# Performance work log

Hardware: AMD Instinct MI355X
Metric: run time of the kernel (lower is better)

Reference implementation:

```python
import jax, jax.numpy as jnp
import numpy as np

N, E, FIN, H, G, L = 100000, 300000, 128, 256, 4000, 5
BN_EPS = 1e-5

def setup_inputs() -> dict:
    key = jax.random.key(0)
    ks = jax.random.split(key, 24)
    s = 0.05
    inp = {
        "x": jax.random.normal(ks[0], (N, FIN), dtype=jnp.float32),
        "edge_index": jax.random.randint(ks[1], (2, E), 0, N, dtype=jnp.int64),
        "batch": jnp.sort(jax.random.randint(ks[2], (N,), 0, G, dtype=jnp.int64)),
        # input projection
        "in_W": jax.random.normal(ks[3], (FIN, H), dtype=jnp.float32) * s,
        "in_b": jnp.zeros((H,), dtype=jnp.float32),
        # stacked per-layer GIN MLP params (Linear-BN-ReLU-Linear-BN-ReLU)
        "conv_W1": jax.random.normal(ks[4], (L, H, H), dtype=jnp.float32) * s,
        "conv_b1": jnp.zeros((L, H), dtype=jnp.float32),
        "conv_g1": jnp.ones((L, H), dtype=jnp.float32),
        "conv_be1": jnp.zeros((L, H), dtype=jnp.float32),
        "conv_W2": jax.random.normal(ks[5], (L, H, H), dtype=jnp.float32) * s,
        "conv_b2": jnp.zeros((L, H), dtype=jnp.float32),
        "conv_g2": jnp.ones((L, H), dtype=jnp.float32),
        "conv_be2": jnp.zeros((L, H), dtype=jnp.float32),
        "eps": jnp.zeros((L,), dtype=jnp.float32),
        # head MLP
        "head_W1": jax.random.normal(ks[6], (H, H // 2), dtype=jnp.float32) * s,
        "head_b1": jnp.zeros((H // 2,), dtype=jnp.float32),
        "head_W2": jax.random.normal(ks[7], (H // 2, 1), dtype=jnp.float32) * s,
        "head_b2": jnp.zeros((1,), dtype=jnp.float32),
    }
    return inp

def _bn(h, g, b):
    # BatchNorm1d over node dim (training-mode batch stats)
    m = jnp.mean(h, axis=0)
    v = jnp.var(h, axis=0)
    return g * (h - m) * jax.lax.rsqrt(v + BN_EPS) + b

def reference(x, edge_index, batch, in_W, in_b, conv_W1, conv_b1, conv_g1,
              conv_be1, conv_W2, conv_b2, conv_g2, conv_be2, eps,
              head_W1, head_b1, head_W2, head_b2):
    src, dst = edge_index[0], edge_index[1]
    h = jax.nn.relu(x @ in_W + in_b)  # [N,H]
    for l in range(L):
        agg = jax.ops.segment_sum(h[src], dst, num_segments=N)  # scatter-add
        z = (1.0 + eps[l]) * h + agg
        z = jax.nn.relu(_bn(z @ conv_W1[l] + conv_b1[l], conv_g1[l], conv_be1[l]))
        h = jax.nn.relu(_bn(z @ conv_W2[l] + conv_b2[l], conv_g2[l], conv_be2[l]))
        # dropout is identity in eval/reference
    # global mean pool by graph id
    sums = jax.ops.segment_sum(h, batch, num_segments=G)  # [G,H]
    cnt = jax.ops.segment_sum(jnp.ones((N,), h.dtype), batch, num_segments=G)
    pooled = sums / jnp.maximum(cnt, 1.0)[:, None]
    hid = jax.nn.relu(pooled @ head_W1 + head_b1)
    return hid @ head_W2 + head_b2  # [G,1]
```

## Files before the change

kernel.cpp:

```cpp
#include <hip/hip_runtime.h>
#include <hip/hip_bf16.h>
#include <stdint.h>
#include <stddef.h>

#define NN 100000
#define NE 300000
#define FINDIM 128
#define HD 256
#define NG 4000
#define NLAYER 5
#define MPAD 100096
#define NT (MPAD/32)
#define MG 384

typedef __attribute__((ext_vector_type(8))) short bf8;
typedef __attribute__((ext_vector_type(4))) float f4;

#define FENCE() __asm__ volatile("" ::: "memory")
#define WAITVM0() __asm__ volatile("s_waitcnt vmcnt(0)" ::: "memory")
#define WAITVM4() __asm__ volatile("s_waitcnt vmcnt(4)" ::: "memory")
#define WAITVM6() __asm__ volatile("s_waitcnt vmcnt(6)" ::: "memory")
#define WAITLGKM() __asm__ volatile("s_waitcnt lgkmcnt(0)" ::: "memory")
#define BARRIER() do { FENCE(); __builtin_amdgcn_s_barrier(); FENCE(); } while(0)

__device__ __forceinline__ unsigned short f2bf(float f){
  union { float f; unsigned u; } uf; uf.f = f;
  unsigned r = uf.u + 0x7fffu + ((uf.u >> 16) & 1u);
  return (unsigned short)(r >> 16);
}
__device__ __forceinline__ float bf2f(unsigned short h){
  union { unsigned u; float f; } uf; uf.u = ((unsigned)h) << 16; return uf.f;
}

__device__ __forceinline__ void gload16(const void* g, void* l){
  __builtin_amdgcn_global_load_lds((const __attribute__((address_space(1))) void*)g,
                                   (__attribute__((address_space(3))) void*)l, 16, 0, 0);
}

__global__ void k_zero(int* __restrict__ p, int n){
  int i = blockIdx.x*256 + threadIdx.x;
  if(i < n) p[i] = 0;
}

__global__ void k_count(const int* __restrict__ ei, int* __restrict__ counts){
  int e = blockIdx.x*256 + threadIdx.x;
  if(e < NE) atomicAdd(&counts[ei[NE + e]], 1);
}

__global__ void k_scan_partial(const int* __restrict__ counts, int* __restrict__ partials){
  __shared__ int sw[4];
  int b = blockIdx.x, t = threadIdx.x;
  int base = b*1024 + t*4;
  int s = 0;
  #pragma unroll
  for(int j=0;j<4;j++){ int i = base+j; if(i < NN) s += counts[i]; }
  #pragma unroll
  for(int d=1; d<64; d<<=1) s += __shfl_xor(s, d, 64);
  if((t & 63) == 0) sw[t>>6] = s;
  __syncthreads();
  if(t == 0) partials[b] = sw[0]+sw[1]+sw[2]+sw[3];
}

__global__ void k_scan_tot(int* __restrict__ partials, int* __restrict__ offsets, int nb){
  __shared__ int sm[128];
  int t = threadIdx.x;
  int v = (t < nb) ? partials[t] : 0;
  sm[t] = v; __syncthreads();
  for(int d=1; d<128; d<<=1){
    int x = 0;
    if(t >= d) x = sm[t-d];
    __syncthreads();
    sm[t] += x;
    __syncthreads();
  }
  if(t < nb) partials[t] = sm[t] - v;
  if(t == 127) offsets[NN] = sm[127];
}

__global__ void k_scan_final(const int* __restrict__ counts, const int* __restrict__ partials,
                             int* __restrict__ offsets, int* __restrict__ cursor){
  __shared__ int wsum[4];
  int b = blockIdx.x, t = threadIdx.x;
  int base = b*1024 + t*4;
  int c[4]; int ts = 0;
  #pragma unroll
  for(int j=0;j<4;j++){ int i = base+j; c[j] = (i < NN) ? counts[i] : 0; ts += c[j]; }
  int lane = t & 63;
  int inc = ts;
  #pragma unroll
  for(int d=1; d<64; d<<=1){ int x = __shfl_up(inc, d, 64); if(lane >= d) inc += x; }
  if(lane == 63) wsum[t>>6] = inc;
  __syncthreads();
  int woff = 0;
  for(int w2=0; w2<(t>>6); w2++) woff += wsum[w2];
  int excl = partials[b] + woff + inc - ts;
  #pragma unroll
  for(int j=0;j<4;j++){
    int i = base+j;
    if(i < NN){ offsets[i] = excl; cursor[i] = excl; excl += c[j]; }
  }
}

__global__ void k_fill(const int* __restrict__ ei, int* __restrict__ cursor, int* __restrict__ eidx){
  int e = blockIdx.x*256 + threadIdx.x;
  if(e < NE){
    int d = ei[NE + e];
    int pos = atomicAdd(&cursor[d], 1);
    eidx[pos] = ei[e];
  }
}

__global__ void k_wt(const float* __restrict__ src, unsigned short* __restrict__ dst, int K, int Ncols){
  int l = blockIdx.y;
  size_t base = (size_t)l * K * Ncols;
  int i = blockIdx.x*256 + threadIdx.x;
  if(i < K*Ncols){
    int k = i / Ncols, n = i % Ncols;
    dst[base + (size_t)n*K + k] = f2bf(src[base + i]);
  }
}

template<int TRANS, bool RELUOUT, bool STATS>
__global__ __launch_bounds__(256, 3) void k_gemmb(
    const unsigned short* __restrict__ A, const unsigned short* __restrict__ Bt,
    const float* __restrict__ bias, const float* __restrict__ preS,
    const float* __restrict__ preT, unsigned short* __restrict__ C,
    float* __restrict__ stats)
{
  __shared__ __align__(16) unsigned short As[2][8192];
  __shared__ __align__(16) unsigned short Cs[4][1152];
  __shared__ __align__(16) float SP[512];
  const int t = threadIdx.x;
  const int lane = t & 63, w = t >> 6;
  const int q = lane >> 4, ln = lane & 15;
  const int nh = blockIdx.x & 1;
  const int mg = blockIdx.x >> 1;
  const int nbase = nh*128 + w*32;

  if(TRANS){ SP[t] = preS[t]; SP[256 + t] = preT[t]; WAITLGKM(); }

  bf8 bb[2][8];
  #pragma unroll
  for(int nf=0; nf<2; nf++)
    #pragma unroll
    for(int s=0; s<8; s++)
      bb[nf][s] = *(const bf8*)(Bt + (size_t)(nbase + nf*16 + ln)*HD + s*32 + q*8);

  float bv[2];
  #pragma unroll
  for(int nf=0; nf<2; nf++) bv[nf] = bias[nbase + nf*16 + ln];

  auto issueA = [&](int mt, int b){
    const int m0 = mt*32;
    #pragma unroll
    for(int j=0; j<4; j++){
      int slot = j*256 + t;
      int row = slot >> 5, p = slot & 31;
      int c = p ^ (row & 7);
      gload16(A + (size_t)(m0 + row)*HD + c*8, &As[b][(j*256 + w*64)*8]);
    }
  };

  float sacc[2] = {0.f, 0.f}, ssacc[2] = {0.f, 0.f};

  issueA(mg, 0);
  issueA(mg + MG, 1);

  int tc = 0;
  for(int mt = mg; mt < NT; mt += MG, tc++){
    const bool last = (mt + MG >= NT);
    if(last)           WAITVM0();
    else if(tc == 0)   WAITVM4();
    else               WAITVM6();
    BARRIER();

    unsigned short* Ab = &As[tc&1][0];
    const int m0 = mt*32;
    const bool padt = (m0 >= NN);

    if(TRANS){
      #pragma unroll
      for(int j=0; j<4; j++){
        int slot = j*256 + t;
        if(padt){
          *(uint4*)&Ab[slot*8] = (uint4){0u,0u,0u,0u};
        } else {
          int row = slot >> 5, p = slot & 31;
          int c = p ^ (row & 7);
          uint4 u = *(const uint4*)&Ab[slot*8];
          f4 s0 = *(const f4*)&SP[c*8];
          f4 s1 = *(const f4*)&SP[c*8 + 4];
          f4 t0 = *(const f4*)&SP[256 + c*8];
          f4 t1 = *(const f4*)&SP[256 + c*8 + 4];
          float scv[8] = {s0.x,s0.y,s0.z,s0.w,s1.x,s1.y,s1.z,s1.w};
          float shv[8] = {t0.x,t0.y,t0.z,t0.w,t1.x,t1.y,t1.z,t1.w};
          unsigned short* us = (unsigned short*)&u;
          #pragma unroll
          for(int e=0; e<8; e++){
            float v = bf2f(us[e]);
            v = fmaxf(fmaf(scv[e], v, shv[e]), 0.f);
            us[e] = f2bf(v);
          }
          *(uint4*)&Ab[slot*8] = u;
        }
      }
      WAITLGKM();
      BARRIER();
    }

    f4 acc[2][2];
    #pragma unroll
    for(int i=0;i<2;i++)
      #pragma unroll
      for(int j=0;j<2;j++) acc[i][j] = (f4){0.f,0.f,0.f,0.f};

    #pragma unroll
    for(int s=0; s<8; s++){
      bf8 af[2];
      #pragma unroll
      for(int mi=0; mi<2; mi++){
        int row = mi*16 + ln;
        int p = (s*4 + q) ^ (row & 7);
        af[mi] = *(const bf8*)&Ab[row*256 + p*8];
      }
      #pragma unroll
      for(int mi=0; mi<2; mi++)
        #pragma unroll
        for(int nf=0; nf<2; nf++)
          acc[mi][nf] = __builtin_amdgcn_mfma_f32_16x16x32_bf16(af[mi], bb[nf][s], acc[mi][nf], 0, 0, 0);
    }

    if(STATS){
      #pragma unroll
      for(int nf=0; nf<2; nf++)
        #pragma unroll
        for(int mi=0; mi<2; mi++)
          #pragma unroll
          for(int r=0; r<4; r++){
            float v = acc[mi][nf][r];
            sacc[nf] += v; ssacc[nf] = fmaf(v, v, ssacc[nf]);
          }
    }

    unsigned short* wsc = &Cs[w][0];
    #pragma unroll
    for(int mi=0; mi<2; mi++)
      #pragma unroll
      for(int nf=0; nf<2; nf++)
        #pragma unroll
        for(int r=0; r<4; r++){
          float v = acc[mi][nf][r] + bv[nf];
          if(RELUOUT) v = fmaxf(v, 0.f);
          if(padt) v = 0.f;
          wsc[(mi*16 + q*4 + r)*36 + nf*16 + ln] = f2bf(v);
        }
    {
      int r2 = lane >> 1, ch = lane & 1;
      size_t cb = (size_t)(m0 + r2)*HD + nh*128 + w*32;
      uint4 u0 = *(const uint4*)&wsc[r2*36 + ch*8];
      uint4 u1 = *(const uint4*)&wsc[r2*36 + (ch+2)*8];
      *(uint4*)&C[cb + ch*8]     = u0;
      *(uint4*)&C[cb + (ch+2)*8] = u1;
    }

    WAITLGKM();
    BARRIER();
    if(mt + 2*MG < NT) issueA(mt + 2*MG, tc&1);
  }

  if(STATS){
    #pragma unroll
    for(int nf=0; nf<2; nf++){
      float s = sacc[nf], ss = ssacc[nf];
      s  += __shfl_xor(s, 16, 64);  s  += __shfl_xor(s, 32, 64);
      ss += __shfl_xor(ss, 16, 64); ss += __shfl_xor(ss, 32, 64);
      if(q == 0){
        int gn = nbase + nf*16 + ln;
        atomicAdd(&stats[gn], s);
        atomicAdd(&stats[HD + gn], ss);
      }
    }
  }
}

__global__ __launch_bounds__(256, 3) void k_gemmb_in(
    const float* __restrict__ A, const unsigned short* __restrict__ Bt,
    const float* __restrict__ bias, unsigned short* __restrict__ C)
{
  __shared__ __align__(16) unsigned short As[4096];
  __shared__ __align__(16) unsigned short Cs[4][1152];
  const int t = threadIdx.x;
  const int lane = t & 63, w = t >> 6;
  const int q = lane >> 4, ln = lane & 15;
  const int nh = blockIdx.x & 1;
  const int mg = blockIdx.x >> 1;
  const int nbase = nh*128 + w*32;

  bf8 bb[2][4];
  #pragma unroll
  for(int nf=0; nf<2; nf++)
    #pragma unroll
    for(int s=0; s<4; s++)
      bb[nf][s] = *(const bf8*)(Bt + (size_t)(nbase + nf*16 + ln)*FINDIM + s*32 + q*8);

  float bv[2];
  #pragma unroll
  for(int nf=0; nf<2; nf++) bv[nf] = bias[nbase + nf*16 + ln];

  for(int mt = mg; mt < NT; mt += MG){
    const int m0 = mt*32;
    const bool padt = (m0 >= NN);
    __syncthreads();
    #pragma unroll
    for(int j=0; j<2; j++){
      int slot = j*256 + t;
      int row = slot >> 4, p = slot & 15;
      int c = p ^ (row & 7);
      int gm = m0 + row;
      f4 v0 = (f4){0.f,0.f,0.f,0.f}, v1 = (f4){0.f,0.f,0.f,0.f};
      if(gm < NN){
        v0 = *(const f4*)&A[(size_t)gm*FINDIM + c*8];
        v1 = *(const f4*)&A[(size_t)gm*FINDIM + c*8 + 4];
      }
      ushort4 a0, a1;
      a0.x = f2bf(v0.x); a0.y = f2bf(v0.y); a0.z = f2bf(v0.z); a0.w = f2bf(v0.w);
      a1.x = f2bf(v1.x); a1.y = f2bf(v1.y); a1.z = f2bf(v1.z); a1.w = f2bf(v1.w);
      *(ushort4*)&As[row*128 + p*8]     = a0;
      *(ushort4*)&As[row*128 + p*8 + 4] = a1;
    }
    __syncthreads();

    f4 acc[2][2];
    #pragma unroll
    for(int i=0;i<2;i++)
      #pragma unroll
      for(int j=0;j<2;j++) acc[i][j] = (f4){0.f,0.f,0.f,0.f};

    #pragma unroll
    for(int s=0; s<4; s++){
      bf8 af[2];
      #pragma unroll
      for(int mi=0; mi<2; mi++){
        int row = mi*16 + ln;
        int p = (s*4 + q) ^ (row & 7);
        af[mi] = *(const bf8*)&As[row*128 + p*8];
      }
      #pragma unroll
      for(int mi=0; mi<2; mi++)
        #pragma unroll
        for(int nf=0; nf<2; nf++)
          acc[mi][nf] = __builtin_amdgcn_mfma_f32_16x16x32_bf16(af[mi], bb[nf][s], acc[mi][nf], 0, 0, 0);
    }

    unsigned short* wsc = &Cs[w][0];
    #pragma unroll
    for(int mi=0; mi<2; mi++)
      #pragma unroll
      for(int nf=0; nf<2; nf++)
        #pragma unroll
        for(int r=0; r<4; r++){
          float v = fmaxf(acc[mi][nf][r] + bv[nf], 0.f);
          if(padt) v = 0.f;
          wsc[(mi*16 + q*4 + r)*36 + nf*16 + ln] = f2bf(v);
        }
    int r2 = lane >> 1, ch = lane & 1;
    size_t cb = (size_t)(m0 + r2)*HD + nh*128 + w*32;
    uint4 u0 = *(const uint4*)&wsc[r2*36 + ch*8];
    uint4 u1 = *(const uint4*)&wsc[r2*36 + (ch+2)*8];
    *(uint4*)&C[cb + ch*8]     = u0;
    *(uint4*)&C[cb + (ch+2)*8] = u1;
  }
}

__global__ void k_bnfin(const float* __restrict__ cs, const float* __restrict__ bias,
                        const float* __restrict__ g, const float* __restrict__ be,
                        float* __restrict__ sc, float* __restrict__ sh){
  int c = threadIdx.x;
  float m0 = cs[c] * (1.0f/NN);
  float mean = m0 + bias[c];
  float var  = cs[HD + c] * (1.0f/NN) - m0*m0;
  float s = g[c] * rsqrtf(var + 1e-5f);
  sc[c] = s;
  sh[c] = be[c] - mean*s;
}

__device__ __forceinline__ f4 act4(ushort4 uv, f4 s4, f4 t4, int ident){
  f4 u;
  u.x = bf2f(uv.x); u.y = bf2f(uv.y); u.z = bf2f(uv.z); u.w = bf2f(uv.w);
  if(!ident){
    u.x = fmaxf(fmaf(s4.x, u.x, t4.x), 0.f);
    u.y = fmaxf(fmaf(s4.y, u.y, t4.y), 0.f);
    u.z = fmaxf(fmaf(s4.z, u.z, t4.z), 0.f);
    u.w = fmaxf(fmaf(s4.w, u.w, t4.w), 0.f);
  }
  return u;
}

__global__ __launch_bounds__(256) void k_agg(const unsigned short* __restrict__ src,
    unsigned short* __restrict__ dst,
    const int* __restrict__ offs, const int* __restrict__ eidx,
    const float* __restrict__ eps, int l,
    const float* __restrict__ sc, const float* __restrict__ sh, int ident)
{
  int wv = threadIdx.x >> 6;
  int n = blockIdx.x*4 + wv;
  if(n >= NN) return;
  int lane = threadIdx.x & 63;
  int c = lane << 2;
  f4 s4 = (f4){0.f,0.f,0.f,0.f}, t4 = (f4){0.f,0.f,0.f,0.f};
  if(!ident){ s4 = *(const f4*)(sc + c); t4 = *(const f4*)(sh + c); }
  float ep = 1.f + eps[l];
  f4 a = act4(*(const ushort4*)(src + (size_t)n*HD + c), s4, t4, ident);
  f4 acc;
  acc.x = ep*a.x; acc.y = ep*a.y; acc.z = ep*a.z; acc.w = ep*a.w;
  int lo = offs[n], hi = offs[n+1];
  for(int base = lo; base < hi; base += 64){
    int rem = hi - base; if(rem > 64) rem = 64;
    int idx = 0;
    if(base + lane < hi) idx = eidx[base + lane];
    int j = 0;
    for(; j + 4 <= rem; j += 4){
      int s0 = __shfl(idx, j, 64),   s1 = __shfl(idx, j+1, 64);
      int s2 = __shfl(idx, j+2, 64), s3 = __shfl(idx, j+3, 64);
      ushort4 u0 = *(const ushort4*)(src + (size_t)s0*HD + c);
      ushort4 u1 = *(const ushort4*)(src + (size_t)s1*HD + c);
      ushort4 u2 = *(const ushort4*)(src + (size_t)s2*HD + c);
      ushort4 u3 = *(const ushort4*)(src + (size_t)s3*HD + c);
      f4 a0 = act4(u0, s4, t4, ident), a1 = act4(u1, s4, t4, ident);
      f4 a2 = act4(u2, s4, t4, ident), a3 = act4(u3, s4, t4, ident);
      acc.x += (a0.x + a1.x) + (a2.x + a3.x);
      acc.y += (a0.y + a1.y) + (a2.y + a3.y);
      acc.z += (a0.z + a1.z) + (a2.z + a3.z);
      acc.w += (a0.w + a1.w) + (a2.w + a3.w);
    }
    for(; j < rem; j++){
      int s0 = __shfl(idx, j, 64);
      f4 a0 = act4(*(const ushort4*)(src + (size_t)s0*HD + c), s4, t4, ident);
      acc.x += a0.x; acc.y += a0.y; acc.z += a0.z; acc.w += a0.w;
    }
  }
  ushort4 o;
  o.x = f2bf(acc.x); o.y = f2bf(acc.y); o.z = f2bf(acc.z); o.w = f2bf(acc.w);
  *(ushort4*)(dst + (size_t)n*HD + c) = o;
}

__device__ __forceinline__ int lowb(const int* __restrict__ arr, int n, int key){
  int lo = 0, hi = n;
  while(lo < hi){ int mid = (lo + hi) >> 1; if(arr[mid] < key) lo = mid + 1; else hi = mid; }
  return lo;
}

__global__ __launch_bounds__(256) void k_pool(const unsigned short* __restrict__ src,
    const int* __restrict__ batch,
    const float* __restrict__ sc, const float* __restrict__ sh, float* __restrict__ pooled)
{
  int wv = threadIdx.x >> 6;
  int g = blockIdx.x*4 + wv;
  if(g >= NG) return;
  int lane = threadIdx.x & 63;
  int c = lane << 2;
  int lo = lowb(batch, NN, g);
  int hi = lowb(batch, NN, g+1);
  f4 s4 = *(const f4*)(sc + c);
  f4 t4 = *(const f4*)(sh + c);
  f4 acc = (f4){0.f,0.f,0.f,0.f};
  for(int n=lo; n<hi; n++){
    ushort4 uv = *(const ushort4*)(src + (size_t)n*HD + c);
    acc.x += fmaxf(fmaf(s4.x, bf2f(uv.x), t4.x), 0.f);
    acc.y += fmaxf(fmaf(s4.y, bf2f(uv.y), t4.y), 0.f);
    acc.z += fmaxf(fmaf(s4.z, bf2f(uv.z), t4.z), 0.f);
    acc.w += fmaxf(fmaf(s4.w, bf2f(uv.w), t4.w), 0.f);
  }
  float inv = 1.0f / fmaxf((float)(hi - lo), 1.0f);
  acc.x *= inv; acc.y *= inv; acc.z *= inv; acc.w *= inv;
  *(f4*)(pooled + (size_t)g*HD + c) = acc;
}

__global__ __launch_bounds__(128) void k_head(const float* __restrict__ pooled,
    const float* __restrict__ W1, const float* __restrict__ b1,
    const float* __restrict__ W2, const float* __restrict__ b2, float* __restrict__ out)
{
  __shared__ float p[HD];
  __shared__ float red[2];
  int g = blockIdx.x, t = threadIdx.x;
  if(t < 64) *(f4*)&p[t*4] = *(const f4*)(pooled + (size_t)g*HD + t*4);
  __syncthreads();
  float s = b1[t];
  for(int k=0;k<HD;k++) s = fmaf(p[k], W1[k*128 + t], s);
  float o = fmaxf(s, 0.f) * W2[t];
  #pragma unroll
  for(int d=1; d<64; d<<=1) o += __shfl_xor(o, d, 64);
  if((t & 63) == 0) red[t>>6] = o;
  __syncthreads();
  if(t == 0) out[g] = red[0] + red[1] + b2[0];
}

extern "C" void kernel_launch(void* const* d_in, const int* in_sizes, int n_in,
                              void* d_out, int out_size, void* d_ws, size_t ws_size,
                              hipStream_t stream) {
  const float* x    = (const float*)d_in[0];
  const int*   ei   = (const int*)  d_in[1];
  const int*   bat  = (const int*)  d_in[2];
  const float* inW  = (const float*)d_in[3];
  const float* inb  = (const float*)d_in[4];
  const float* W1   = (const float*)d_in[5];
  const float* b1   = (const float*)d_in[6];
  const float* g1   = (const float*)d_in[7];
  const float* be1  = (const float*)d_in[8];
  const float* W2   = (const float*)d_in[9];
  const float* b2   = (const float*)d_in[10];
  const float* g2   = (const float*)d_in[11];
  const float* be2  = (const float*)d_in[12];
  const float* eps  = (const float*)d_in[13];
  const float* hW1  = (const float*)d_in[14];
  const float* hb1  = (const float*)d_in[15];
  const float* hW2  = (const float*)d_in[16];
  const float* hb2  = (const float*)d_in[17];
  float* out = (float*)d_out;

  char* p = (char*)d_ws;
  auto alloc = [&](size_t bytes)->char*{
    char* r = p; p += (bytes + 255) & ~(size_t)255; return r;
  };
  unsigned short* B0 = (unsigned short*)alloc((size_t)MPAD*HD*2);
  unsigned short* B1 = (unsigned short*)alloc((size_t)MPAD*HD*2);
  unsigned short* Wtin = (unsigned short*)alloc((size_t)FINDIM*HD*2);
  unsigned short* Wt1  = (unsigned short*)alloc((size_t)NLAYER*HD*HD*2);
  unsigned short* Wt2  = (unsigned short*)alloc((size_t)NLAYER*HD*HD*2);
  int* counts  = (int*)alloc((size_t)NN*4);
  int* offsets = (int*)alloc((size_t)(NN+1)*4);
  int* cursor  = (int*)alloc((size_t)NN*4);
  int* eidx    = (int*)alloc((size_t)NE*4);
  int* partials= (int*)alloc(128*4);
  float* cs    = (float*)alloc(4*HD*4);
  float* bnp   = (float*)alloc(4*HD*4);
  float* pooled= (float*)alloc((size_t)NG*HD*4);

  k_zero<<<(NN+255)/256, 256, 0, stream>>>(counts, NN);
  k_count<<<(NE+255)/256, 256, 0, stream>>>(ei, counts);
  int nb = (NN + 1023)/1024;
  k_scan_partial<<<nb, 256, 0, stream>>>(counts, partials);
  k_scan_tot<<<1, 128, 0, stream>>>(partials, offsets, nb);
  k_scan_final<<<nb, 256, 0, stream>>>(counts, partials, offsets, cursor);
  k_fill<<<(NE+255)/256, 256, 0, stream>>>(ei, cursor, eidx);

  k_wt<<<dim3((FINDIM*HD+255)/256, 1), 256, 0, stream>>>(inW, Wtin, FINDIM, HD);
  k_wt<<<dim3((HD*HD+255)/256, NLAYER), 256, 0, stream>>>(W1, Wt1, HD, HD);
  k_wt<<<dim3((HD*HD+255)/256, NLAYER), 256, 0, stream>>>(W2, Wt2, HD, HD);

  {
    int padInts = (MPAD - NN) * HD / 2;
    k_zero<<<(padInts+255)/256, 256, 0, stream>>>((int*)(B1 + (size_t)NN*HD), padInts);
  }

  k_gemmb_in<<<2*MG, 256, 0, stream>>>(x, Wtin, inb, B0);

  float* sc1 = bnp, *sh1 = bnp + HD, *sc2 = bnp + 2*HD, *sh2 = bnp + 3*HD;
  unsigned short* hbuf = B0;
  unsigned short* tbuf = B1;
  for(int l=0; l<NLAYER; l++){
    k_zero<<<4, 256, 0, stream>>>((int*)cs, 4*HD);
    k_agg<<<(NN+3)/4, 256, 0, stream>>>(hbuf, tbuf, offsets, eidx, eps, l, sc2, sh2, l==0 ? 1 : 0);
    k_gemmb<0, false, true><<<2*MG, 256, 0, stream>>>(tbuf, Wt1 + (size_t)l*HD*HD, b1 + l*HD,
                                                      nullptr, nullptr, hbuf, cs);
    k_bnfin<<<1, HD, 0, stream>>>(cs, b1 + l*HD, g1 + l*HD, be1 + l*HD, sc1, sh1);
    k_gemmb<1, false, true><<<2*MG, 256, 0, stream>>>(hbuf, Wt2 + (size_t)l*HD*HD, b2 + l*HD,
                                                      sc1, sh1, tbuf, cs + 2*HD);
    k_bnfin<<<1, HD, 0, stream>>>(cs + 2*HD, b2 + l*HD, g2 + l*HD, be2 + l*HD, sc2, sh2);
    unsigned short* tmp = hbuf; hbuf = tbuf; tbuf = tmp;
  }

  k_pool<<<(NG+3)/4, 256, 0, stream>>>(hbuf, bat, sc2, sh2, pooled);
  k_head<<<NG, 128, 0, stream>>>(pooled, hW1, hb1, hW2, hb2, out);
}
```

Baseline: 836.0 us.

## Restructure GEMMs into per-wave 16-row tiles with 64-column slices

```diff
diff --git a/kernel.cpp b/kernel.cpp
--- a/kernel.cpp
+++ b/kernel.cpp
@@ -10,18 +10,17 @@
 #define NG 4000
 #define NLAYER 5
 #define MPAD 100096
-#define NT (MPAD/32)
-#define MG 384
+#define NT16 (MPAD/16)
+#define NSTR 512
+#define NREM (NT16 - 12*NSTR)
 
 typedef __attribute__((ext_vector_type(8))) short bf8;
 typedef __attribute__((ext_vector_type(4))) float f4;
 
-#define FENCE() __asm__ volatile("" ::: "memory")
-#define WAITVM0() __asm__ volatile("s_waitcnt vmcnt(0)" ::: "memory")
-#define WAITVM4() __asm__ volatile("s_waitcnt vmcnt(4)" ::: "memory")
-#define WAITVM6() __asm__ volatile("s_waitcnt vmcnt(6)" ::: "memory")
+#define WAITVM2()  __asm__ volatile("s_waitcnt vmcnt(2)" ::: "memory")
+#define WAITVM8()  __asm__ volatile("s_waitcnt vmcnt(8)" ::: "memory")
+#define WAITVM10() __asm__ volatile("s_waitcnt vmcnt(10)" ::: "memory")
 #define WAITLGKM() __asm__ volatile("s_waitcnt lgkmcnt(0)" ::: "memory")
-#define BARRIER() do { FENCE(); __builtin_amdgcn_s_barrier(); FENCE(); } while(0)
 
 __device__ __forceinline__ unsigned short f2bf(float f){
   union { float f; unsigned u; } uf; uf.f = f;
@@ -121,156 +120,143 @@
 }
 
 template<int TRANS, bool RELUOUT, bool STATS>
-__global__ __launch_bounds__(256, 3) void k_gemmb(
+__global__ __launch_bounds__(256, 2) void k_gemmb(
     const unsigned short* __restrict__ A, const unsigned short* __restrict__ Bt,
     const float* __restrict__ bias, const float* __restrict__ preS,
     const float* __restrict__ preT, unsigned short* __restrict__ C,
     float* __restrict__ stats)
 {
-  __shared__ __align__(16) unsigned short As[2][8192];
-  __shared__ __align__(16) unsigned short Cs[4][1152];
-  __shared__ __align__(16) float SP[512];
+  __shared__ __align__(16) unsigned short As[4][2][4096];
+  __shared__ __align__(16) unsigned short Cs[4][1120];
   const int t = threadIdx.x;
   const int lane = t & 63, w = t >> 6;
   const int q = lane >> 4, ln = lane & 15;
-  const int nh = blockIdx.x & 1;
-  const int mg = blockIdx.x >> 1;
-  const int nbase = nh*128 + w*32;
-
-  if(TRANS){ SP[t] = preS[t]; SP[256 + t] = preT[t]; WAITLGKM(); }
-
-  bf8 bb[2][8];
-  #pragma unroll
-  for(int nf=0; nf<2; nf++)
+  const int pl = lane & 31, rh = lane >> 5;
+  const int g  = blockIdx.x & 3;
+  const int mg = blockIdx.x >> 2;
+  const int sid = mg*4 + w;
+  const int nbase = g*64;
+
+  bf8 bb[4][8];
+  #pragma unroll
+  for(int nf=0; nf<4; nf++)
     #pragma unroll
     for(int s=0; s<8; s++)
       bb[nf][s] = *(const bf8*)(Bt + (size_t)(nbase + nf*16 + ln)*HD + s*32 + q*8);
 
-  float bv[2];
-  #pragma unroll
-  for(int nf=0; nf<2; nf++) bv[nf] = bias[nbase + nf*16 + ln];
+  float bv[4];
+  #pragma unroll
+  for(int nf=0; nf<4; nf++) bv[nf] = bias[nbase + nf*16 + ln];
+
+  f4 sA={0.f,0.f,0.f,0.f}, sB=sA, tA=sA, tB=sA;
+  if(TRANS){
+    sA = *(const f4*)(preS + pl*8);  sB = *(const f4*)(preS + pl*8 + 4);
+    tA = *(const f4*)(preT + pl*8);  tB = *(const f4*)(preT + pl*8 + 4);
+  }
 
   auto issueA = [&](int mt, int b){
-    const int m0 = mt*32;
-    #pragma unroll
-    for(int j=0; j<4; j++){
-      int slot = j*256 + t;
-      int row = slot >> 5, p = slot & 31;
-      int c = p ^ (row & 7);
-      gload16(A + (size_t)(m0 + row)*HD + c*8, &As[b][(j*256 + w*64)*8]);
+    const int m0 = mt*16;
+    #pragma unroll
+    for(int j=0; j<8; j++){
+      int row = j*2 + rh;
+      int c = pl ^ (row & 7);
+      gload16(A + (size_t)(m0 + row)*HD + c*8, &As[w][b][j*512]);
     }
   };
 
-  float sacc[2] = {0.f, 0.f}, ssacc[2] = {0.f, 0.f};
-
-  issueA(mg, 0);
-  issueA(mg + MG, 1);
-
-  int tc = 0;
-  for(int mt = mg; mt < NT; mt += MG, tc++){
-    const bool last = (mt + MG >= NT);
-    if(last)           WAITVM0();
-    else if(tc == 0)   WAITVM4();
-    else               WAITVM6();
-    BARRIER();
-
-    unsigned short* Ab = &As[tc&1][0];
-    const int m0 = mt*32;
+  const int nt = (sid < NREM) ? 13 : 12;
+  issueA(sid, 0);
+  issueA(sid + NSTR, 1);
+
+  float sacc[4] = {0.f,0.f,0.f,0.f}, ssacc[4] = {0.f,0.f,0.f,0.f};
+
+  for(int k=0; k<nt; k++){
+    const int mt = sid + k*NSTR;
+    const int m0 = mt*16;
+    const int buf = k & 1;
+    if(k == 0)            WAITVM8();
+    else if(k == nt-1)    WAITVM2();
+    else                  WAITVM10();
+
+    unsigned short* Ab = &As[w][buf][0];
     const bool padt = (m0 >= NN);
+    if(padt){
+      uint4 z = (uint4){0u,0u,0u,0u};
+      int r2 = lane >> 2, sg = lane & 3;
+      size_t cb = (size_t)(m0 + r2)*HD + nbase;
+      *(uint4*)&C[cb + sg*8]     = z;
+      *(uint4*)&C[cb + (sg+4)*8] = z;
+      continue;
+    }
 
     if(TRANS){
       #pragma unroll
-      for(int j=0; j<4; j++){
-        int slot = j*256 + t;
-        if(padt){
-          *(uint4*)&Ab[slot*8] = (uint4){0u,0u,0u,0u};
-        } else {
-          int row = slot >> 5, p = slot & 31;
-          int c = p ^ (row & 7);
-          uint4 u = *(const uint4*)&Ab[slot*8];
-          f4 s0 = *(const f4*)&SP[c*8];
-          f4 s1 = *(const f4*)&SP[c*8 + 4];
-          f4 t0 = *(const f4*)&SP[256 + c*8];
-          f4 t1 = *(const f4*)&SP[256 + c*8 + 4];
-          float scv[8] = {s0.x,s0.y,s0.z,s0.w,s1.x,s1.y,s1.z,s1.w};
-          float shv[8] = {t0.x,t0.y,t0.z,t0.w,t1.x,t1.y,t1.z,t1.w};
-          unsigned short* us = (unsigned short*)&u;
-          #pragma unroll
-          for(int e=0; e<8; e++){
-            float v = bf2f(us[e]);
-            v = fmaxf(fmaf(scv[e], v, shv[e]), 0.f);
-            us[e] = f2bf(v);
-          }
-          *(uint4*)&Ab[slot*8] = u;
+      for(int j=0; j<8; j++){
+        int row = rh*8 + j;
+        int p = pl ^ (row & 7);
+        uint4 u = *(uint4*)&Ab[row*256 + p*8];
+        unsigned short* us = (unsigned short*)&u;
+        #pragma unroll
+        for(int e=0; e<8; e++){
+          float sc = (e<4) ? sA[e] : sB[e-4];
+          float sh = (e<4) ? tA[e] : tB[e-4];
+          float v = bf2f(us[e]);
+          v = fmaxf(fmaf(sc, v, sh), 0.f);
+          us[e] = f2bf(v);
         }
+        *(uint4*)&Ab[row*256 + p*8] = u;
       }
-      WAITLGKM();
-      BARRIER();
-    }
-
-    f4 acc[2][2];
-    #pragma unroll
-    for(int i=0;i<2;i++)
-      #pragma unroll
-      for(int j=0;j<2;j++) acc[i][j] = (f4){0.f,0.f,0.f,0.f};
-
+    }
+
+    f4 acc[4];
+    #pragma unroll
+    for(int nf=0; nf<4; nf++) acc[nf] = (f4){0.f,0.f,0.f,0.f};
+
+    __builtin_amdgcn_s_setprio(1);
     #pragma unroll
     for(int s=0; s<8; s++){
-      bf8 af[2];
-      #pragma unroll
-      for(int mi=0; mi<2; mi++){
-        int row = mi*16 + ln;
-        int p = (s*4 + q) ^ (row & 7);
-        af[mi] = *(const bf8*)&Ab[row*256 + p*8];
-      }
-      #pragma unroll
-      for(int mi=0; mi<2; mi++)
-        #pragma unroll
-        for(int nf=0; nf<2; nf++)
-          acc[mi][nf] = __builtin_amdgcn_mfma_f32_16x16x32_bf16(af[mi], bb[nf][s], acc[mi][nf], 0, 0, 0);
-    }
+      bf8 af = *(const bf8*)&Ab[ln*256 + ((s*4 + q) ^ (ln & 7))*8];
+      #pragma unroll
+      for(int nf=0; nf<4; nf++)
+        acc[nf] = __builtin_amdgcn_mfma_f32_16x16x32_bf16(af, bb[nf][s], acc[nf], 0, 0, 0);
+    }
+    __builtin_amdgcn_s_setprio(0);
 
     if(STATS){
       #pragma unroll
-      for(int nf=0; nf<2; nf++)
-        #pragma unroll
-        for(int mi=0; mi<2; mi++)
-          #pragma unroll
-          for(int r=0; r<4; r++){
-            float v = acc[mi][nf][r];
-            sacc[nf] += v; ssacc[nf] = fmaf(v, v, ssacc[nf]);
-          }
-    }
-
-    unsigned short* wsc = &Cs[w][0];
-    #pragma unroll
-    for(int mi=0; mi<2; mi++)
-      #pragma unroll
-      for(int nf=0; nf<2; nf++)
+      for(int nf=0; nf<4; nf++)
         #pragma unroll
         for(int r=0; r<4; r++){
-          float v = acc[mi][nf][r] + bv[nf];
-          if(RELUOUT) v = fmaxf(v, 0.f);
-          if(padt) v = 0.f;
-          wsc[(mi*16 + q*4 + r)*36 + nf*16 + ln] = f2bf(v);
+          float v = acc[nf][r];
+          sacc[nf] += v; ssacc[nf] = fmaf(v, v, ssacc[nf]);
         }
+    }
+
+    unsigned short* wsc = &Cs[w][0];
+    #pragma unroll
+    for(int nf=0; nf<4; nf++)
+      #pragma unroll
+      for(int r=0; r<4; r++){
+        float v = acc[nf][r] + bv[nf];
+        if(RELUOUT) v = fmaxf(v, 0.f);
+        wsc[(q*4 + r)*70 + nf*16 + ln] = f2bf(v);
+      }
     {
-      int r2 = lane >> 1, ch = lane & 1;
-      size_t cb = (size_t)(m0 + r2)*HD + nh*128 + w*32;
-      uint4 u0 = *(const uint4*)&wsc[r2*36 + ch*8];
-      uint4 u1 = *(const uint4*)&wsc[r2*36 + (ch+2)*8];
-      *(uint4*)&C[cb + ch*8]     = u0;
-      *(uint4*)&C[cb + (ch+2)*8] = u1;
+      int r2 = lane >> 2, sg = lane & 3;
+      size_t cb = (size_t)(m0 + r2)*HD + nbase;
+      uint4 u0 = *(const uint4*)&wsc[r2*70 + sg*8];
+      uint4 u1 = *(const uint4*)&wsc[r2*70 + (sg+4)*8];
+      *(uint4*)&C[cb + sg*8]     = u0;
+      *(uint4*)&C[cb + (sg+4)*8] = u1;
     }
 
     WAITLGKM();
-    BARRIER();
-    if(mt + 2*MG < NT) issueA(mt + 2*MG, tc&1);
+    if(k + 2 < nt) issueA(sid + (k+2)*NSTR, buf);
   }
 
   if(STATS){
     #pragma unroll
-    for(int nf=0; nf<2; nf++){
+    for(int nf=0; nf<4; nf++){
       float s = sacc[nf], ss = ssacc[nf];
       s  += __shfl_xor(s, 16, 64);  s  += __shfl_xor(s, 32, 64);
       ss += __shfl_xor(ss, 16, 64); ss += __shfl_xor(ss, 32, 64);
@@ -283,92 +269,109 @@
   }
 }
 
-__global__ __launch_bounds__(256, 3) void k_gemmb_in(
+__global__ __launch_bounds__(256, 2) void k_gemmb_in(
     const float* __restrict__ A, const unsigned short* __restrict__ Bt,
     const float* __restrict__ bias, unsigned short* __restrict__ C)
 {
-  __shared__ __align__(16) unsigned short As[4096];
-  __shared__ __align__(16) unsigned short Cs[4][1152];
+  __shared__ __align__(16) unsigned short As[4][2048];
+  __shared__ __align__(16) unsigned short Cs[4][1120];
   const int t = threadIdx.x;
   const int lane = t & 63, w = t >> 6;
   const int q = lane >> 4, ln = lane & 15;
-  const int nh = blockIdx.x & 1;
-  const int mg = blockIdx.x >> 1;
-  const int nbase = nh*128 + w*32;
-
-  bf8 bb[2][4];
-  #pragma unroll
-  for(int nf=0; nf<2; nf++)
+  const int g  = blockIdx.x & 3;
+  const int mg = blockIdx.x >> 2;
+  const int sid = mg*4 + w;
+  const int nbase = g*64;
+
+  bf8 bb[4][4];
+  #pragma unroll
+  for(int nf=0; nf<4; nf++)
     #pragma unroll
     for(int s=0; s<4; s++)
       bb[nf][s] = *(const bf8*)(Bt + (size_t)(nbase + nf*16 + ln)*FINDIM + s*32 + q*8);
 
-  float bv[2];
-  #pragma unroll
-  for(int nf=0; nf<2; nf++) bv[nf] = bias[nbase + nf*16 + ln];
-
-  for(int mt = mg; mt < NT; mt += MG){
-    const int m0 = mt*32;
+  float bv[4];
+  #pragma unroll
+  for(int nf=0; nf<4; nf++) bv[nf] = bias[nbase + nf*16 + ln];
+
+  const int nt = (sid < NREM) ? 13 : 12;
+
+  auto loadT = [&](int mt, f4 (&r)[8]){
+    const int m0 = mt*16;
+    #pragma unroll
+    for(int m=0; m<4; m++){
+      int row = m*4 + (lane >> 4);
+      int c = (lane & 15) ^ (row & 7);
+      int gm = m0 + row;
+      f4 v0 = (f4){0.f,0.f,0.f,0.f}, v1 = v0;
+      if(gm < NN){
+        v0 = *(const f4*)(A + (size_t)gm*FINDIM + c*8);
+        v1 = *(const f4*)(A + (size_t)gm*FINDIM + c*8 + 4);
+      }
+      r[2*m] = v0; r[2*m+1] = v1;
+    }
+  };
+
+  auto body = [&](int k, f4 (&rg)[8]){
+    const int mt = sid + k*NSTR;
+    const int m0 = mt*16;
     const bool padt = (m0 >= NN);
-    __syncthreads();
-    #pragma unroll
-    for(int j=0; j<2; j++){
-      int slot = j*256 + t;
-      int row = slot >> 4, p = slot & 15;
-      int c = p ^ (row & 7);
-      int gm = m0 + row;
-      f4 v0 = (f4){0.f,0.f,0.f,0.f}, v1 = (f4){0.f,0.f,0.f,0.f};
-      if(gm < NN){
-        v0 = *(const f4*)&A[(size_t)gm*FINDIM + c*8];
-        v1 = *(const f4*)&A[(size_t)gm*FINDIM + c*8 + 4];
+    if(!padt){
+      #pragma unroll
+      for(int m=0; m<4; m++){
+        int row = m*4 + (lane >> 4);
+        int p = lane & 15;
+        ushort4 h0, h1;
+        h0.x = f2bf(rg[2*m].x);   h0.y = f2bf(rg[2*m].y);
+        h0.z = f2bf(rg[2*m].z);   h0.w = f2bf(rg[2*m].w);
+        h1.x = f2bf(rg[2*m+1].x); h1.y = f2bf(rg[2*m+1].y);
+        h1.z = f2bf(rg[2*m+1].z); h1.w = f2bf(rg[2*m+1].w);
+        *(ushort4*)&As[w][row*128 + p*8]     = h0;
+        *(ushort4*)&As[w][row*128 + p*8 + 4] = h1;
       }
-      ushort4 a0, a1;
-      a0.x = f2bf(v0.x); a0.y = f2bf(v0.y); a0.z = f2bf(v0.z); a0.w = f2bf(v0.w);
-      a1.x = f2bf(v1.x); a1.y = f2bf(v1.y); a1.z = f2bf(v1.z); a1.w = f2bf(v1.w);
-      *(ushort4*)&As[row*128 + p*8]     = a0;
-      *(ushort4*)&As[row*128 + p*8 + 4] = a1;
-    }
-    __syncthreads();
-
-    f4 acc[2][2];
-    #pragma unroll
-    for(int i=0;i<2;i++)
-      #pragma unroll
-      for(int j=0;j<2;j++) acc[i][j] = (f4){0.f,0.f,0.f,0.f};
-
+    }
+    if(k + 2 < nt) loadT(sid + (k+2)*NSTR, rg);
+    int r2 = lane >> 2, sg = lane & 3;
+    size_t cb = (size_t)(m0 + r2)*HD + nbase;
+    if(padt){
+      uint4 z = (uint4){0u,0u,0u,0u};
+      *(uint4*)&C[cb + sg*8]     = z;
+      *(uint4*)&C[cb + (sg+4)*8] = z;
+      return;
+    }
+    f4 acc[4];
+    #pragma unroll
+    for(int nf=0; nf<4; nf++) acc[nf] = (f4){0.f,0.f,0.f,0.f};
+    __builtin_amdgcn_s_setprio(1);
     #pragma unroll
     for(int s=0; s<4; s++){
-      bf8 af[2];
-      #pragma unroll
-      for(int mi=0; mi<2; mi++){
-        int row = mi*16 + ln;
-        int p = (s*4 + q) ^ (row & 7);
-        af[mi] = *(const bf8*)&As[row*128 + p*8];
+      bf8 af = *(const bf8*)&As[w][ln*128 + ((s*4 + q) ^ (ln & 7))*8];
+      #pragma unroll
+      for(int nf=0; nf<4; nf++)
+        acc[nf] = __builtin_amdgcn_mfma_f32_16x16x32_bf16(af, bb[nf][s], acc[nf], 0, 0, 0);
+    }
+    __builtin_amdgcn_s_setprio(0);
+    unsigned short* wsc = &Cs[w][0];
+    #pragma unroll
+    for(int nf=0; nf<4; nf++)
+      #pragma unroll
+      for(int r=0; r<4; r++){
+        float v = fmaxf(acc[nf][r] + bv[nf], 0.f);
+        wsc[(q*4 + r)*70 + nf*16 + ln] = f2bf(v);
       }
-      #pragma unroll
-      for(int mi=0; mi<2; mi++)
-        #pragma unroll
-        for(int nf=0; nf<2; nf++)
-          acc[mi][nf] = __builtin_amdgcn_mfma_f32_16x16x32_bf16(af[mi], bb[nf][s], acc[mi][nf], 0, 0, 0);
-    }
-
-    unsigned short* wsc = &Cs[w][0];
-    #pragma unroll
-    for(int mi=0; mi<2; mi++)
-      #pragma unroll
-      for(int nf=0; nf<2; nf++)
-        #pragma unroll
-        for(int r=0; r<4; r++){
-          float v = fmaxf(acc[mi][nf][r] + bv[nf], 0.f);
-          if(padt) v = 0.f;
-          wsc[(mi*16 + q*4 + r)*36 + nf*16 + ln] = f2bf(v);
-        }
-    int r2 = lane >> 1, ch = lane & 1;
-    size_t cb = (size_t)(m0 + r2)*HD + nh*128 + w*32;
-    uint4 u0 = *(const uint4*)&wsc[r2*36 + ch*8];
-    uint4 u1 = *(const uint4*)&wsc[r2*36 + (ch+2)*8];
-    *(uint4*)&C[cb + ch*8]     = u0;
-    *(uint4*)&C[cb + (ch+2)*8] = u1;
+    uint4 u0 = *(const uint4*)&wsc[r2*70 + sg*8];
+    uint4 u1 = *(const uint4*)&wsc[r2*70 + (sg+4)*8];
+    *(uint4*)&C[cb + sg*8]     = u0;
+    *(uint4*)&C[cb + (sg+4)*8] = u1;
+  };
+
+  f4 ra[8], rb[8];
+  loadT(sid, ra);
+  loadT(sid + NSTR, rb);
+  int k = 0;
+  for(;;){
+    body(k, ra); if(++k >= nt) break;
+    body(k, rb); if(++k >= nt) break;
   }
 }
 
@@ -553,7 +556,7 @@
     k_zero<<<(padInts+255)/256, 256, 0, stream>>>((int*)(B1 + (size_t)NN*HD), padInts);
   }
 
-  k_gemmb_in<<<2*MG, 256, 0, stream>>>(x, Wtin, inb, B0);
+  k_gemmb_in<<<512, 256, 0, stream>>>(x, Wtin, inb, B0);
 
   float* sc1 = bnp, *sh1 = bnp + HD, *sc2 = bnp + 2*HD, *sh2 = bnp + 3*HD;
   unsigned short* hbuf = B0;
@@ -561,11 +564,11 @@
   for(int l=0; l<NLAYER; l++){
     k_zero<<<4, 256, 0, stream>>>((int*)cs, 4*HD);
     k_agg<<<(NN+3)/4, 256, 0, stream>>>(hbuf, tbuf, offsets, eidx, eps, l, sc2, sh2, l==0 ? 1 : 0);
-    k_gemmb<0, false, true><<<2*MG, 256, 0, stream>>>(tbuf, Wt1 + (size_t)l*HD*HD, b1 + l*HD,
-                                                      nullptr, nullptr, hbuf, cs);
+    k_gemmb<0, false, true><<<512, 256, 0, stream>>>(tbuf, Wt1 + (size_t)l*HD*HD, b1 + l*HD,
+                                                     nullptr, nullptr, hbuf, cs);
     k_bnfin<<<1, HD, 0, stream>>>(cs, b1 + l*HD, g1 + l*HD, be1 + l*HD, sc1, sh1);
-    k_gemmb<1, false, true><<<2*MG, 256, 0, stream>>>(hbuf, Wt2 + (size_t)l*HD*HD, b2 + l*HD,
-                                                      sc1, sh1, tbuf, cs + 2*HD);
+    k_gemmb<1, false, true><<<512, 256, 0, stream>>>(hbuf, Wt2 + (size_t)l*HD*HD, b2 + l*HD,
+                                                     sc1, sh1, tbuf, cs + 2*HD);
     k_bnfin<<<1, HD, 0, stream>>>(cs + 2*HD, b2 + l*HD, g2 + l*HD, be2 + l*HD, sc2, sh2);
     unsigned short* tmp = hbuf; hbuf = tbuf; tbuf = tmp;
   }
```

New measurement: 998.7 us. +19.5%, slower.

## Triple-buffer A tiles, drop end-of-iteration barrier, hold BN scale/shift in registers

Applied to the files above, without the earlier changes.

```diff
diff --git a/kernel.cpp b/kernel.cpp
--- a/kernel.cpp
+++ b/kernel.cpp
@@ -17,7 +17,7 @@
 typedef __attribute__((ext_vector_type(4))) float f4;
 
 #define FENCE() __asm__ volatile("" ::: "memory")
-#define WAITVM0() __asm__ volatile("s_waitcnt vmcnt(0)" ::: "memory")
+#define WAITVM2() __asm__ volatile("s_waitcnt vmcnt(2)" ::: "memory")
 #define WAITVM4() __asm__ volatile("s_waitcnt vmcnt(4)" ::: "memory")
 #define WAITVM6() __asm__ volatile("s_waitcnt vmcnt(6)" ::: "memory")
 #define WAITLGKM() __asm__ volatile("s_waitcnt lgkmcnt(0)" ::: "memory")
@@ -127,9 +127,8 @@
     const float* __restrict__ preT, unsigned short* __restrict__ C,
     float* __restrict__ stats)
 {
-  __shared__ __align__(16) unsigned short As[2][8192];
-  __shared__ __align__(16) unsigned short Cs[4][1152];
-  __shared__ __align__(16) float SP[512];
+  __shared__ __align__(16) unsigned short As[3][8192];
+  __shared__ __align__(16) unsigned short Cs[4][576];
   const int t = threadIdx.x;
   const int lane = t & 63, w = t >> 6;
   const int q = lane >> 4, ln = lane & 15;
@@ -137,8 +136,6 @@
   const int mg = blockIdx.x >> 1;
   const int nbase = nh*128 + w*32;
 
-  if(TRANS){ SP[t] = preS[t]; SP[256 + t] = preT[t]; WAITLGKM(); }
-
   bf8 bb[2][8];
   #pragma unroll
   for(int nf=0; nf<2; nf++)
@@ -149,6 +146,13 @@
   float bv[2];
   #pragma unroll
   for(int nf=0; nf<2; nf++) bv[nf] = bias[nbase + nf*16 + ln];
+
+  f4 sA = (f4){0.f,0.f,0.f,0.f}, sB = sA, tA = sA, tB = sA;
+  if(TRANS){
+    int cc = (t & 31) * 8;
+    sA = *(const f4*)(preS + cc);  sB = *(const f4*)(preS + cc + 4);
+    tA = *(const f4*)(preT + cc);  tB = *(const f4*)(preT + cc + 4);
+  }
 
   auto issueA = [&](int mt, int b){
     const int m0 = mt*32;
@@ -166,106 +170,101 @@
   issueA(mg, 0);
   issueA(mg + MG, 1);
 
-  int tc = 0;
-  for(int mt = mg; mt < NT; mt += MG, tc++){
+  int k = 0;
+  for(int mt = mg; mt < NT; mt += MG, k++){
     const bool last = (mt + MG >= NT);
-    if(last)           WAITVM0();
-    else if(tc == 0)   WAITVM4();
-    else               WAITVM6();
+    if(last)        WAITVM2();
+    else if(k == 0) WAITVM4();
+    else            WAITVM6();
     BARRIER();
 
-    unsigned short* Ab = &As[tc&1][0];
+    unsigned short* Ab = &As[k % 3][0];
     const int m0 = mt*32;
     const bool padt = (m0 >= NN);
 
-    if(TRANS){
-      #pragma unroll
-      for(int j=0; j<4; j++){
-        int slot = j*256 + t;
-        if(padt){
-          *(uint4*)&Ab[slot*8] = (uint4){0u,0u,0u,0u};
-        } else {
-          int row = slot >> 5, p = slot & 31;
-          int c = p ^ (row & 7);
-          uint4 u = *(const uint4*)&Ab[slot*8];
-          f4 s0 = *(const f4*)&SP[c*8];
-          f4 s1 = *(const f4*)&SP[c*8 + 4];
-          f4 t0 = *(const f4*)&SP[256 + c*8];
-          f4 t1 = *(const f4*)&SP[256 + c*8 + 4];
-          float scv[8] = {s0.x,s0.y,s0.z,s0.w,s1.x,s1.y,s1.z,s1.w};
-          float shv[8] = {t0.x,t0.y,t0.z,t0.w,t1.x,t1.y,t1.z,t1.w};
+    if(padt){
+      uint4 z = (uint4){0u,0u,0u,0u};
+      int r2 = lane >> 2, sg = lane & 3;
+      *(uint4*)&C[(size_t)(m0 + r2)*HD + nbase + sg*8]      = z;
+      *(uint4*)&C[(size_t)(m0 + 16 + r2)*HD + nbase + sg*8] = z;
+    } else {
+      if(TRANS){
+        const int r0 = t >> 5;
+        const int p  = (t & 31) ^ r0;
+        #pragma unroll
+        for(int i=0; i<4; i++){
+          int row = r0 + 8*i;
+          uint4 u = *(uint4*)&Ab[(row*32 + p)*8];
           unsigned short* us = (unsigned short*)&u;
           #pragma unroll
           for(int e=0; e<8; e++){
+            float sc = (e<4) ? sA[e] : sB[e-4];
+            float sh = (e<4) ? tA[e] : tB[e-4];
             float v = bf2f(us[e]);
-            v = fmaxf(fmaf(scv[e], v, shv[e]), 0.f);
+            v = fmaxf(fmaf(sc, v, sh), 0.f);
             us[e] = f2bf(v);
           }
-          *(uint4*)&Ab[slot*8] = u;
+          *(uint4*)&Ab[(row*32 + p)*8] = u;
         }
-      }
-      WAITLGKM();
-      BARRIER();
-    }
-
-    f4 acc[2][2];
-    #pragma unroll
-    for(int i=0;i<2;i++)
-      #pragma unroll
-      for(int j=0;j<2;j++) acc[i][j] = (f4){0.f,0.f,0.f,0.f};
-
-    #pragma unroll
-    for(int s=0; s<8; s++){
-      bf8 af[2];
-      #pragma unroll
-      for(int mi=0; mi<2; mi++){
-        int row = mi*16 + ln;
-        int p = (s*4 + q) ^ (row & 7);
-        af[mi] = *(const bf8*)&Ab[row*256 + p*8];
-      }
-      #pragma unroll
-      for(int mi=0; mi<2; mi++)
-        #pragma unroll
-        for(int nf=0; nf<2; nf++)
-          acc[mi][nf] = __builtin_amdgcn_mfma_f32_16x16x32_bf16(af[mi], bb[nf][s], acc[mi][nf], 0, 0, 0);
-    }
-
-    if(STATS){
-      #pragma unroll
-      for(int nf=0; nf<2; nf++)
+        WAITLGKM();
+        BARRIER();
+      }
+
+      f4 acc[2][2];
+      #pragma unroll
+      for(int i=0;i<2;i++)
+        #pragma unroll
+        for(int j=0;j<2;j++) acc[i][j] = (f4){0.f,0.f,0.f,0.f};
+
+      __builtin_amdgcn_s_setprio(1);
+      #pragma unroll
+      for(int s=0; s<8; s++){
+        bf8 af[2];
+        #pragma unroll
+        for(int mi=0; mi<2; mi++){
+          int row = mi*16 + ln;
+          int p = (s*4 + q) ^ (row & 7);
+          af[mi] = *(const bf8*)&Ab[row*256 + p*8];
+        }
         #pragma unroll
         for(int mi=0; mi<2; mi++)
           #pragma unroll
+          for(int nf=0; nf<2; nf++)
+            acc[mi][nf] = __builtin_amdgcn_mfma_f32_16x16x32_bf16(af[mi], bb[nf][s], acc[mi][nf], 0, 0, 0);
+      }
+      __builtin_amdgcn_s_setprio(0);
+
+      if(STATS){
+        #pragma unroll
+        for(int nf=0; nf<2; nf++)
+          #pragma unroll
+          for(int mi=0; mi<2; mi++)
+            #pragma unroll
+            for(int r=0; r<4; r++){
+              float v = acc[mi][nf][r];
+              sacc[nf] += v; ssacc[nf] = fmaf(v, v, ssacc[nf]);
+            }
+      }
+
+      unsigned short* wsc = &Cs[w][0];
+      #pragma unroll
+      for(int mi=0; mi<2; mi++){
+        #pragma unroll
+        for(int nf=0; nf<2; nf++)
+          #pragma unroll
           for(int r=0; r<4; r++){
-            float v = acc[mi][nf][r];
-            sacc[nf] += v; ssacc[nf] = fmaf(v, v, ssacc[nf]);
+            float v = acc[mi][nf][r] + bv[nf];
+            if(RELUOUT) v = fmaxf(v, 0.f);
+            wsc[(q*4 + r)*36 + nf*16 + ln] = f2bf(v);
           }
-    }
-
-    unsigned short* wsc = &Cs[w][0];
-    #pragma unroll
-    for(int mi=0; mi<2; mi++)
-      #pragma unroll
-      for(int nf=0; nf<2; nf++)
-        #pragma unroll
-        for(int r=0; r<4; r++){
-          float v = acc[mi][nf][r] + bv[nf];
-          if(RELUOUT) v = fmaxf(v, 0.f);
-          if(padt) v = 0.f;
-          wsc[(mi*16 + q*4 + r)*36 + nf*16 + ln] = f2bf(v);
-        }
-    {
-      int r2 = lane >> 1, ch = lane & 1;
-      size_t cb = (size_t)(m0 + r2)*HD + nh*128 + w*32;
-      uint4 u0 = *(const uint4*)&wsc[r2*36 + ch*8];
-      uint4 u1 = *(const uint4*)&wsc[r2*36 + (ch+2)*8];
-      *(uint4*)&C[cb + ch*8]     = u0;
-      *(uint4*)&C[cb + (ch+2)*8] = u1;
-    }
-
-    WAITLGKM();
-    BARRIER();
-    if(mt + 2*MG < NT) issueA(mt + 2*MG, tc&1);
+        int r2 = lane >> 2, sg = lane & 3;
+        uint4 u = *(const uint4*)&wsc[r2*36 + sg*8];
+        *(uint4*)&C[(size_t)(m0 + mi*16 + r2)*HD + nbase + sg*8] = u;
+      }
+    }
+
+    FENCE();
+    if(mt + 2*MG < NT) issueA(mt + 2*MG, (k+2) % 3);
   }
 
   if(STATS){
```

Result: faster. 811.0 us (-3.0%).
